# Kernel tuning notes

Measured on AMD Instinct MI355X. Metric: run time of the kernel, lower is better.

The kernel has to match this reference:

```python
import jax, jax.numpy as jnp
import numpy as np

jax.config.update("jax_enable_x64", True)  # hash uses int64 multiply-xor like torch .long()

NUM_LEVELS = 16
LEVEL_DIM = 2
PER_LEVEL_SCALE = 2
BASE_RES = 16
LOG2_HASHMAP = 19
PS1 = 19349663  # second spatial hash prime (ps[0] == 1)
N_POINTS = 524288


def _isprime(n):
    for p in range(2, int(n ** 0.5) + 1):
        if n % p == 0:
            return False
    return True


N_ENTRIES = 2 ** LOG2_HASHMAP
while not _isprime(N_ENTRIES):
    N_ENTRIES += 1  # -> 524309

SCALES = []
OFFSETS = [0]
START_HASH = NUM_LEVELS  # module uses -1 sentinel; NUM_LEVELS == 'no hashing yet'
for i in range(NUM_LEVELS):
    res = int(BASE_RES * PER_LEVEL_SCALE ** i)
    SCALES.append(res)
    n = (res + 1) ** 2
    if n > N_ENTRIES:
        if START_HASH == NUM_LEVELS:
            START_HASH = i
        n = N_ENTRIES
    OFFSETS.append(OFFSETS[-1] + n)
TABLE_SIZE = OFFSETS[-1]  # 5594552

CORNERS = jnp.array([[0.0, 0.0], [0.0, 1.0], [1.0, 0.0], [1.0, 1.0]], dtype=jnp.float32)  # [4,2]
SCALES_F = jnp.array(SCALES, dtype=jnp.float32)          # [L]
SCALES_I = jnp.array(SCALES, dtype=jnp.int64)            # [L]
LEVEL_OFF = jnp.array(OFFSETS[:-1], dtype=jnp.int64)     # [L] base offset per level


def setup_inputs() -> dict:
    key = jax.random.key(0)
    k1, k2 = jax.random.split(key)
    x = jax.random.uniform(k1, (N_POINTS, 2), dtype=jnp.float32)  # coords in [0,1)
    data = (jax.random.uniform(k2, (TABLE_SIZE, LEVEL_DIM), dtype=jnp.float32) * 2.0 - 1.0) * 1e-4
    return {"x": x, "data": data}


def reference(x, data):
    L, F = NUM_LEVELS, LEVEL_DIM
    float_x = x[None] * SCALES_F[:, None, None]                                  # [L,N,2]
    int_x = (float_x[:, :, None, :] + CORNERS[None, None]).astype(jnp.int64)     # [L,N,4,2]
    offset_x = float_x - int_x[:, :, 0].astype(float_x.dtype)                    # [L,N,2] frac part
    ix0, ix1 = int_x[..., 0], int_x[..., 1]
    # dense-grid index for low levels, spatial hash for high levels
    grid_ind = ix0 * (SCALES_I + 1)[:, None, None] + ix1                         # [L,N,4]
    hash_ind = (ix0 ^ (ix1 * PS1)) % N_ENTRIES                                   # [L,N,4]
    is_grid = (jnp.arange(L) < START_HASH)[:, None, None]
    ind = jnp.where(is_grid, grid_ind, hash_ind) + LEVEL_OFF[:, None, None]      # [L,N,4]
    val = data[ind]                                                              # [L,N,4,F]
    # bilinear corner weights: clamp(1 - c + (2c-1)*frac) per axis, product over xy
    w = jnp.clip(1.0 - CORNERS[None, None] + (2.0 * CORNERS[None, None] - 1.0) * offset_x[:, :, None], 0.0, 1.0)
    w = w[..., 0] * w[..., 1]                                                    # [L,N,4]
    out = jnp.einsum('lnc,lncf->lnf', w, val)                                    # [L,N,F]
    return out.transpose(1, 0, 2).reshape(-1, L * F)                             # [N, L*F]
```

## Files before the change

kernel.cpp:

```cpp
#include <hip/hip_runtime.h>


static constexpr int  kPoints    = 524288;
static constexpr int  kLevels    = 16;
static constexpr int  kStartHash = 6;
static constexpr long long kPs1     = 19349663LL;
static constexpr long long kEntries = 524309LL;

__constant__ long long c_level_off[kLevels] = {
    0LL, 289LL, 1378LL, 5603LL, 22244LL, 88293LL, 351462LL,
    875771LL, 1400080LL, 1924389LL, 2448698LL, 2973007LL,
    3497316LL, 4021625LL, 4545934LL, 5070243LL
};

__device__ __forceinline__ float2 interp_level(
    const float2 p, const float2* __restrict__ tbl, const int l)
{
    const int   scale_i = 16 << l;
    const float scale_f = (float)scale_i;

    const float fx = p.x * scale_f;
    const float fy = p.y * scale_f;

    const long long ix0 = (long long)fx;
    const long long iy0 = (long long)fy;
    const long long ix1 = (long long)(fx + 1.0f);
    const long long iy1 = (long long)(fy + 1.0f);

    const float ox = fx - (float)ix0;
    const float oy = fy - (float)iy0;

    const float wx1 = fminf(fmaxf(ox, 0.0f), 1.0f);
    const float wx0 = fminf(fmaxf(1.0f - ox, 0.0f), 1.0f);
    const float wy1 = fminf(fmaxf(oy, 0.0f), 1.0f);
    const float wy0 = fminf(fmaxf(1.0f - oy, 0.0f), 1.0f);

    long long i00, i01, i10, i11;
    if (l < kStartHash) {
        const long long stride = (long long)(scale_i + 1);
        i00 = ix0 * stride + iy0;
        i01 = ix0 * stride + iy1;
        i10 = ix1 * stride + iy0;
        i11 = ix1 * stride + iy1;
    } else {
        const long long hy0 = iy0 * kPs1;
        const long long hy1 = iy1 * kPs1;
        i00 = (ix0 ^ hy0) % kEntries;
        i01 = (ix0 ^ hy1) % kEntries;
        i10 = (ix1 ^ hy0) % kEntries;
        i11 = (ix1 ^ hy1) % kEntries;
    }

    const long long base = c_level_off[l];
    const float2 v00 = tbl[base + i00];
    const float2 v01 = tbl[base + i01];
    const float2 v10 = tbl[base + i10];
    const float2 v11 = tbl[base + i11];

    const float w00 = wx0 * wy0;
    const float w01 = wx0 * wy1;
    const float w10 = wx1 * wy0;
    const float w11 = wx1 * wy1;

    return make_float2(
        w00 * v00.x + w01 * v01.x + w10 * v10.x + w11 * v11.x,
        w00 * v00.y + w01 * v01.y + w10 * v10.y + w11 * v11.y);
}

__global__ __launch_bounds__(256) void level_pass(
    const float2* __restrict__ x,
    const float2* __restrict__ tbl,
    float2* __restrict__ ws)
{
    const int l = blockIdx.x >> 11;
    const int n = ((blockIdx.x & 2047) << 8) | threadIdx.x;
    const float2 p = x[n];
    ws[(size_t)l * kPoints + n] = interp_level(p, tbl, l);
}

__global__ __launch_bounds__(256) void gather_out(
    const float2* __restrict__ ws,
    float4* __restrict__ out)
{
    const int f = blockIdx.x * 256 + threadIdx.x;
    const int n = f >> 3;
    const int i = f & 7;
    const float2 a = ws[(size_t)(2 * i)     * kPoints + n];
    const float2 b = ws[(size_t)(2 * i + 1) * kPoints + n];
    out[f] = make_float4(a.x, a.y, b.x, b.y);
}

__global__ __launch_bounds__(256) void hashgrid_fwd(
    const float2* __restrict__ x,
    const float2* __restrict__ tbl,
    float4* __restrict__ out)
{
    const int n = blockIdx.x * blockDim.x + threadIdx.x;
    if (n >= kPoints) return;
    const float2 p = x[n];
    float acc[2 * kLevels];
#pragma unroll
    for (int l = 0; l < kLevels; ++l) {
        const float2 r = interp_level(p, tbl, l);
        acc[2 * l + 0] = r.x;
        acc[2 * l + 1] = r.y;
    }
    float4* o = out + (size_t)n * 8;
#pragma unroll
    for (int i = 0; i < 8; ++i)
        o[i] = make_float4(acc[4 * i + 0], acc[4 * i + 1],
                           acc[4 * i + 2], acc[4 * i + 3]);
}

extern "C" void kernel_launch(void* const* d_in, const int* in_sizes, int n_in,
                              void* d_out, int out_size, void* d_ws, size_t ws_size,
                              hipStream_t stream) {
    const float2* x   = (const float2*)d_in[0];
    const float2* tbl = (const float2*)d_in[1];

    const size_t ws_needed = (size_t)kLevels * kPoints * sizeof(float2);
    if (ws_size >= ws_needed) {
        float2* ws = (float2*)d_ws;
        level_pass<<<kLevels * (kPoints / 256), 256, 0, stream>>>(x, tbl, ws);
        gather_out<<<(kPoints * 8) / 256, 256, 0, stream>>>(ws, (float4*)d_out);
    } else {
        hashgrid_fwd<<<kPoints / 256, 256, 0, stream>>>(x, tbl, (float4*)d_out);
    }
}
```

Before: 227.6 us.

## Pin hashed levels to XCDs for L2 locality and transpose output via LDS

Block indices in the level pass are remapped so each of the 8 XCDs owns one hashed level (6-13). Levels 14 and 15 are split evenly across the XCDs, and the dense levels are spread out as well. The aim is to keep each 4 MB hash-table slice resident in a single XCD's L2 instead of every XCD thrashing over all levels. The gather kernel becomes an LDS-staged transpose with a padded stride, so workspace reads are coalesced per level. This depends on blocks being dispatched round-robin across XCDs.

```diff
diff --git a/kernel.cpp b/kernel.cpp
--- a/kernel.cpp
+++ b/kernel.cpp
@@ -72,22 +72,58 @@
     const float2* __restrict__ tbl,
     float2* __restrict__ ws)
 {
-    const int l = blockIdx.x >> 11;
-    const int n = ((blockIdx.x & 2047) << 8) | threadIdx.x;
+    const int b    = blockIdx.x;
+    const int xcd  = b & 7;
+    const int slot = b >> 3;
+
+    int level, pblk;
+    if (slot < 2048) {
+        level = 6 + xcd;
+        pblk  = slot;
+    } else if (slot < 2304) {
+        level = 14;
+        pblk  = xcd * 256 + (slot - 2048);
+    } else if (slot < 2560) {
+        level = 15;
+        pblk  = xcd * 256 + (slot - 2304);
+    } else {
+        const int d = xcd * 1536 + (slot - 2560);
+        level = d >> 11;
+        pblk  = d & 2047;
+    }
+
+    const int n = (pblk << 8) | threadIdx.x;
     const float2 p = x[n];
-    ws[(size_t)l * kPoints + n] = interp_level(p, tbl, l);
+    ws[(size_t)level * kPoints + n] = interp_level(p, tbl, level);
 }
 
-__global__ __launch_bounds__(256) void gather_out(
+static constexpr int kTStride = 257;
+
+__global__ __launch_bounds__(256) void transpose_out(
     const float2* __restrict__ ws,
     float4* __restrict__ out)
 {
-    const int f = blockIdx.x * 256 + threadIdx.x;
-    const int n = f >> 3;
-    const int i = f & 7;
-    const float2 a = ws[(size_t)(2 * i)     * kPoints + n];
-    const float2 b = ws[(size_t)(2 * i + 1) * kPoints + n];
-    out[f] = make_float4(a.x, a.y, b.x, b.y);
+    __shared__ float2 lds[kLevels * kTStride];
+
+    const int t  = threadIdx.x;
+    const int n0 = blockIdx.x * 256;
+
+#pragma unroll
+    for (int l = 0; l < kLevels; ++l)
+        lds[l * kTStride + t] = ws[(size_t)l * kPoints + n0 + t];
+
+    __syncthreads();
+
+    float4* o = out + (size_t)n0 * 8;
+#pragma unroll
+    for (int k = 0; k < 8; ++k) {
+        const int f  = k * 256 + t;
+        const int nl = f >> 3;
+        const int i  = t & 7;
+        const float2 a = lds[(2 * i)     * kTStride + nl];
+        const float2 b = lds[(2 * i + 1) * kTStride + nl];
+        o[f] = make_float4(a.x, a.y, b.x, b.y);
+    }
 }
 
 __global__ __launch_bounds__(256) void hashgrid_fwd(
@@ -122,7 +158,7 @@
     if (ws_size >= ws_needed) {
         float2* ws = (float2*)d_ws;
         level_pass<<<kLevels * (kPoints / 256), 256, 0, stream>>>(x, tbl, ws);
-        gather_out<<<(kPoints * 8) / 256, 256, 0, stream>>>(ws, (float4*)d_out);
+        transpose_out<<<kPoints / 256, 256, 0, stream>>>(ws, (float4*)d_out);
     } else {
         hashgrid_fwd<<<kPoints / 256, 256, 0, stream>>>(x, tbl, (float4*)d_out);
     }
```

After: 227.0 us. Within noise of the previous version (-0.3%).
